# Kernel optimization log

Measured on AMD Instinct MI355X. Metric: run time of the kernel, lower is better.

The kernel has to match this reference:

```python
import jax, jax.numpy as jnp
import numpy as np

N, E, X_DIM, EA_DIM, HID, NL, NC, NGRAPH = 50000, 800000, 64, 16, 64, 3, 10, 64
BN_EPS = 1e-5
STD_EPS = 1e-5


def setup_inputs() -> dict:
    key = jax.random.key(0)
    ks = jax.random.split(key, 24)
    w = lambda k, sh: (jax.random.normal(k, sh, jnp.float32) * 0.05)
    inp = {
        'x': jax.random.normal(ks[0], (N, X_DIM), jnp.float32),
        'edge_index': jax.random.randint(ks[1], (2, E), 0, N),
        'batch': jnp.sort(jax.random.randint(ks[2], (N,), 0, NGRAPH)),
        'edge_attr': jax.random.normal(ks[3], (E, EA_DIM), jnp.float32),
        # node / edge encoders
        'node_w': w(ks[4], (X_DIM, HID)), 'node_b': jnp.zeros((HID,), jnp.float32),
        'edge_w': w(ks[5], (EA_DIM, HID)), 'edge_b': jnp.zeros((HID,), jnp.float32),
        # per-layer PNA post_nn Linear(12*3*HID -> HID) and BatchNorm
        'conv_w': w(ks[6], (NL, 12 * 3 * HID, HID)), 'conv_b': jnp.zeros((NL, HID), jnp.float32),
        'bn_g': jnp.ones((NL, HID), jnp.float32), 'bn_b': jnp.zeros((NL, HID), jnp.float32),
        # fc_out: HID -> HID/2 -> HID/4 -> NC
        'fc1_w': w(ks[7], (HID, HID // 2)), 'fc1_b': jnp.zeros((HID // 2,), jnp.float32),
        'fc2_w': w(ks[8], (HID // 2, HID // 4)), 'fc2_b': jnp.zeros((HID // 4,), jnp.float32),
        'fc3_w': w(ks[9], (HID // 4, NC)), 'fc3_b': jnp.zeros((NC,), jnp.float32),
    }
    return inp


def _pna_layer(x, src, dst, ea, deg, degc, log_deg, avg_log, w, b):
    # message: concat([x_i, x_j, edge_attr]) with x_i = x[dst], x_j = x[src]  -> [E, 3H]
    h = jnp.concatenate([x[dst], x[src], ea], axis=-1)
    inv = (1.0 / degc)[:, None]
    s1 = jax.ops.segment_sum(h, dst, num_segments=N)
    mean = s1 * inv
    mean_sq = jax.ops.segment_sum(h * h, dst, num_segments=N) * inv
    std = jnp.sqrt(jax.nn.relu(mean_sq - mean * mean) + STD_EPS)
    has = (deg > 0)[:, None]
    mx = jax.ops.segment_max(h, dst, num_segments=N)
    mx = jnp.where(has, mx, 0.0)
    mn = -jax.ops.segment_max(-h, dst, num_segments=N)
    mn = jnp.where(has, mn, 0.0)
    out = jnp.concatenate([mean, mn, mx, std], axis=-1)  # [N, 4*3H]
    amp = (log_deg / avg_log)[:, None]
    att = (avg_log / log_deg)[:, None]
    out = jnp.concatenate([out, out * amp, out * att], axis=-1)  # [N, 12*3H]
    return out @ w + b


def reference(x, edge_index, batch, edge_attr, node_w, node_b, edge_w, edge_b,
              conv_w, conv_b, bn_g, bn_b, fc1_w, fc1_b, fc2_w, fc2_b, fc3_w, fc3_b):
    src, dst = edge_index[0], edge_index[1]
    x = x @ node_w + node_b
    ea = edge_attr @ edge_w + edge_b
    deg = jax.ops.segment_sum(jnp.ones((E,), jnp.float32), dst, num_segments=N)
    degc = jnp.maximum(deg, 1.0)
    log_deg = jnp.log(degc + 1.0)
    # avg of log(deg+1) over nodes (equivalent to the histogram-based avg_deg['log'])
    avg_log = jnp.mean(jnp.log(deg + 1.0))
    for i in range(NL):
        h = _pna_layer(x, src, dst, ea, deg, degc, log_deg, avg_log, conv_w[i], conv_b[i])
        mu = jnp.mean(h, axis=0)
        var = jnp.mean((h - mu) ** 2, axis=0)  # biased var, as torch BN training mode
        h = (h - mu) * jax.lax.rsqrt(var + BN_EPS) * bn_g[i] + bn_b[i]
        x = jax.nn.relu(h) + x  # dropout is identity in eval
    # global mean pool over graphs
    gsum = jax.ops.segment_sum(x, batch, num_segments=NGRAPH)
    gcnt = jnp.maximum(jax.ops.segment_sum(jnp.ones((N,), jnp.float32), batch, num_segments=NGRAPH), 1.0)
    g = gsum / gcnt[:, None]
    g = jax.nn.relu(g @ fc1_w + fc1_b)
    g = jax.nn.relu(g @ fc2_w + fc2_b)
    return g @ fc3_w + fc3_b
```

## Files before the change

kernel.cpp:

```cpp
#include <hip/hip_runtime.h>
#include <math.h>

#define N_NODES 50000
#define N_EDGES 800000
#define NGRAPH  64
#define KEFF    576

typedef short bf16x8 __attribute__((ext_vector_type(8)));
typedef float f32x4  __attribute__((ext_vector_type(4)));
typedef unsigned int u32;
typedef unsigned int u32x4 __attribute__((ext_vector_type(4)));

__device__ inline unsigned short f2bf_rne(float f) {
  unsigned u = __float_as_uint(f);
  unsigned r = u + 0x7FFFu + ((u >> 16) & 1u);
  return (unsigned short)(r >> 16);
}
__device__ inline float bf2f(unsigned short h) {
  return __uint_as_float(((unsigned)h) << 16);
}

__device__ inline u32 cvtpk_bf16(float a, float b) {
  u32 r;
  asm("v_cvt_pk_bf16_f32 %0, %1, %2" : "=v"(r) : "v"(a), "v"(b));
  return r;
}

__device__ inline void split2(float a, float b, u32& ph, u32& pl) {
  ph = cvtpk_bf16(a, b);
  float ha = __uint_as_float(ph << 16);
  float hb = __uint_as_float(ph & 0xFFFF0000u);
  pl = cvtpk_bf16(a - ha, b - hb);
}

__device__ inline bf16x8 pack_bf(u32 w0, u32 w1, u32 w2, u32 w3) {
  u32x4 t;
  t.x = w0; t.y = w1; t.z = w2; t.w = w3;
  return __builtin_bit_cast(bf16x8, t);
}


__global__ __launch_bounds__(256) void zero_kernel(
    int* __restrict__ cnt, float* __restrict__ gsum,
    double* __restrict__ bnacc, double* __restrict__ avgacc)
{
  int i = blockIdx.x * 256 + threadIdx.x;
  if (i < N_NODES) { cnt[i] = 0; return; }
  int j = i - N_NODES;
  if (j < NGRAPH * 64) { gsum[j] = 0.f; return; }
  int k = j - NGRAPH * 64;
  if (k < 3 * 128) { bnacc[k] = 0.0; return; }
  if (k == 3 * 128) *avgacc = 0.0;
}

__global__ __launch_bounds__(256) void node_enc_kernel(
    const float* __restrict__ xin, const float* __restrict__ nw,
    const float* __restrict__ nb, float* __restrict__ x)
{
  __shared__ float xs[256];
  int tid = threadIdx.x;
  int base = blockIdx.x * 256;
  xs[tid] = xin[base + tid];
  __syncthreads();
  int r = tid >> 6, j = tid & 63;
  float acc = nb[j];
#pragma unroll
  for (int t = 0; t < 64; t++) acc = fmaf(xs[r * 64 + t], nw[t * 64 + j], acc);
  x[base + tid] = acc;
}

__global__ void count_kernel(const int* __restrict__ dst, int* __restrict__ cnt)
{
  int e = blockIdx.x * 256 + threadIdx.x;
  atomicAdd(&cnt[dst[e]], 1);
}

__global__ __launch_bounds__(256) void scan_a_kernel(
    const int* __restrict__ cnt, int* __restrict__ bsum)
{
  __shared__ int s[256];
  int i = blockIdx.x * 256 + threadIdx.x;
  s[threadIdx.x] = (i < N_NODES) ? cnt[i] : 0;
  __syncthreads();
  for (int off = 128; off > 0; off >>= 1) {
    if (threadIdx.x < off) s[threadIdx.x] += s[threadIdx.x + off];
    __syncthreads();
  }
  if (threadIdx.x == 0) bsum[blockIdx.x] = s[0];
}

__global__ __launch_bounds__(256) void scan_b_kernel(
    const int* __restrict__ bsum, int* __restrict__ boff)
{
  __shared__ int s[256];
  int tid = threadIdx.x;
  int v = (tid < 196) ? bsum[tid] : 0;
  s[tid] = v;
  __syncthreads();
  for (int off = 1; off < 256; off <<= 1) {
    int t = (tid >= off) ? s[tid - off] : 0;
    __syncthreads();
    s[tid] += t;
    __syncthreads();
  }
  boff[tid] = s[tid] - v;
}

__global__ __launch_bounds__(256) void scan_c_kernel(
    const int* __restrict__ cnt, const int* __restrict__ boff,
    int* __restrict__ row_ptr, int* __restrict__ cursor)
{
  __shared__ int s[256];
  int tid = threadIdx.x;
  int i = blockIdx.x * 256 + tid;
  int v = (i < N_NODES) ? cnt[i] : 0;
  s[tid] = v;
  __syncthreads();
  for (int off = 1; off < 256; off <<= 1) {
    int t = (tid >= off) ? s[tid - off] : 0;
    __syncthreads();
    s[tid] += t;
    __syncthreads();
  }
  int incl = s[tid];
  int base = boff[blockIdx.x];
  if (i < N_NODES) { row_ptr[i] = base + incl - v; cursor[i] = base + incl - v; }
  if (i == N_NODES - 1) row_ptr[N_NODES] = base + incl;
}

__global__ void fill_kernel(const int* __restrict__ src, const int* __restrict__ dst,
                            int* __restrict__ cursor, int* __restrict__ srcs,
                            int* __restrict__ eids)
{
  int e = blockIdx.x * 256 + threadIdx.x;
  int d = dst[e];
  int pos = atomicAdd(&cursor[d], 1);
  srcs[pos] = src[e];
  eids[pos] = e;
}

__global__ __launch_bounds__(256) void deg_log_kernel(
    const int* __restrict__ cnt, float* __restrict__ log_deg,
    double* __restrict__ avgacc)
{
  __shared__ double sb[256];
  int i = blockIdx.x * 256 + threadIdx.x;
  double c = 0.0;
  if (i < N_NODES) {
    int d = cnt[i];
    int dc = d > 0 ? d : 1;
    log_deg[i] = logf((float)dc + 1.0f);
    c = (double)logf((float)d + 1.0f);
  }
  sb[threadIdx.x] = c;
  __syncthreads();
  for (int off = 128; off > 0; off >>= 1) {
    if (threadIdx.x < off) sb[threadIdx.x] += sb[threadIdx.x + off];
    __syncthreads();
  }
  if (threadIdx.x == 0) atomicAdd(avgacc, sb[0]);
}

__global__ void avg_gb_kernel(const double* __restrict__ avgacc,
                              float* __restrict__ avgf,
                              const int* __restrict__ batch,
                              int* __restrict__ gcnt)
{
  __shared__ int sb[65];
  int g = threadIdx.x;
  int lo = 0, hi = N_NODES;
  while (lo < hi) { int mid = (lo + hi) >> 1; if (batch[mid] < g) lo = mid + 1; else hi = mid; }
  sb[g] = lo;
  if (g == 0) { sb[64] = N_NODES; *avgf = (float)(*avgacc / (double)N_NODES); }
  __syncthreads();
  gcnt[g] = sb[g + 1] - sb[g];
}


__global__ __launch_bounds__(256) void wprep_kernel(
    const float* __restrict__ conv_w, unsigned short* __restrict__ wh,
    unsigned short* __restrict__ wl)
{
  int idx = blockIdx.x * 256 + threadIdx.x;
  int k = idx % 576;
  int c = (idx / 576) % 192;
  int l = idx / (576 * 192);
  int s = c >> 6, j = c & 63;
  const float* CW = conv_w + (size_t)l * 2304 * 64;
  float v;
  if (k < 64) {
    int base = s * 768 + k;
    v = CW[base * 64 + j] + CW[(base + 192) * 64 + j] + CW[(base + 384) * 64 + j];
  } else {
    const int srcseg[8] = {1, 2, 4, 5, 7, 8, 10, 11};
    int q = (k >> 6) - 1;
    int t = k & 63;
    v = CW[(s * 768 + srcseg[q] * 64 + t) * 64 + j];
  }
  unsigned short hh = f2bf_rne(v);
  size_t o = (((size_t)l * 12 + (c >> 4)) * 72 + (k >> 3)) * 128 + (c & 15) * 8 + (k & 7);
  wh[o] = hh;
  wl[o] = f2bf_rne(v - bf2f(hh));
}

__global__ void bprep_kernel(const float* __restrict__ conv_w, float* __restrict__ beff)
{
  int l = blockIdx.x;
  int s = threadIdx.x >> 6, j = threadIdx.x & 63;
  const float* CW = conv_w + (size_t)l * 2304 * 64 + (size_t)(s * 768 + 576) * 64;
  float sum = 0.f;
#pragma unroll
  for (int t = 0; t < 64; t++) sum += CW[t * 64 + j];
  beff[(l * 3 + s) * 64 + j] = sum * 0.0031622776601683794f;
}

__global__ __launch_bounds__(256) void ewprep_kernel(
    const float* __restrict__ edge_w, unsigned short* __restrict__ ewh,
    unsigned short* __restrict__ ewl)
{
  int tid = threadIdx.x;
#pragma unroll
  for (int it = 0; it < 4; it++) {
    int idx = tid + 256 * it;
    int j = idx & 7, cb = (idx >> 3) & 3, l15 = (idx >> 5) & 15, hf = idx >> 9;
    float v = edge_w[(hf * 8 + j) * 64 + cb * 16 + l15];
    unsigned short h = f2bf_rne(v);
    ewh[idx] = h;
    ewl[idx] = f2bf_rne(v - bf2f(h));
  }
}


__device__ inline bf16x8 load_afrag(const float* __restrict__ eattr,
                                    const int* __restrict__ eids,
                                    int idx, int quad, bool wantlo)
{
  int eid = eids[idx];
  const float4* rp = (const float4*)(eattr + (size_t)eid * 16 + (quad & 1) * 8);
  float4 r0 = rp[0], r1 = rp[1];
  u32 h0, l0, h1, l1, h2, l2, h3, l3;
  split2(r0.x, r0.y, h0, l0);
  split2(r0.z, r0.w, h1, l1);
  split2(r1.x, r1.y, h2, l2);
  split2(r1.z, r1.w, h3, l3);
  return pack_bf(wantlo ? l0 : h0, wantlo ? l1 : h1,
                 wantlo ? l2 : h2, wantlo ? l3 : h3);
}

#define AGG_E_BLOCKS 2048
#define AGG_E_WAVES  (AGG_E_BLOCKS * 4)

__global__ __launch_bounds__(256) void agg_e_kernel(
    const float* __restrict__ eattr,
    const unsigned short* __restrict__ ewh, const unsigned short* __restrict__ ewl,
    const float* __restrict__ edge_b, const int* __restrict__ row_ptr,
    const int* __restrict__ eids,
    unsigned short* __restrict__ agg_h, unsigned short* __restrict__ agg_l)
{
  int lane = threadIdx.x & 63;
  int quad = lane >> 4, l15 = lane & 15;
  bool wantlo = quad >= 2;
  float eb = edge_b[lane];

  int fbase = ((quad & 1) * 16 + l15) * 32;
  bf16x8 wbh[4], wbl[4];
#pragma unroll
  for (int cb = 0; cb < 4; cb++) {
    wbh[cb] = *(const bf16x8*)(ewh + fbase + cb * 8);
    wbl[cb] = *(const bf16x8*)(ewl + fbase + cb * 8);
  }

  const f32x4 zero = {};
  for (int n = blockIdx.x * 4 + (threadIdx.x >> 6); n < N_NODES; n += AGG_E_WAVES) {
    int s0 = row_ptr[n], s1 = row_ptr[n + 1];
    float se[4] = {0.f, 0.f, 0.f, 0.f}, sq[4] = {0.f, 0.f, 0.f, 0.f};
    float mx[4], mn[4];
#pragma unroll
    for (int cb = 0; cb < 4; cb++) { mx[cb] = -3.4e38f; mn[cb] = 3.4e38f; }

    int j = s0;
    for (; j + 16 <= s1; j += 16) {
      bf16x8 af = load_afrag(eattr, eids, j + l15, quad, wantlo);
#pragma unroll
      for (int cb = 0; cb < 4; cb++) {
        f32x4 acc = __builtin_amdgcn_mfma_f32_16x16x32_bf16(af, wbh[cb], zero, 0, 0, 0);
        acc = __builtin_amdgcn_mfma_f32_16x16x32_bf16(af, wbl[cb], acc, 0, 0, 0);
#pragma unroll
        for (int r = 0; r < 4; r++) {
          float v = acc[r];
          se[cb] += v; sq[cb] = fmaf(v, v, sq[cb]);
          mx[cb] = fmaxf(mx[cb], v); mn[cb] = fminf(mn[cb], v);
        }
      }
    }
    if (j < s1) {
      int rem = s1 - j;
      int idx = j + l15; if (idx > s1 - 1) idx = s1 - 1;
      bf16x8 af = load_afrag(eattr, eids, idx, quad, wantlo);
#pragma unroll
      for (int cb = 0; cb < 4; cb++) {
        f32x4 acc = __builtin_amdgcn_mfma_f32_16x16x32_bf16(af, wbh[cb], zero, 0, 0, 0);
        acc = __builtin_amdgcn_mfma_f32_16x16x32_bf16(af, wbl[cb], acc, 0, 0, 0);
#pragma unroll
        for (int r = 0; r < 4; r++) {
          float v = acc[r];
          bool valid = (quad * 4 + r) < rem;
          float vm = valid ? v : 0.f;
          se[cb] += vm; sq[cb] = fmaf(vm, vm, sq[cb]);
          mx[cb] = fmaxf(mx[cb], v); mn[cb] = fminf(mn[cb], v);
        }
      }
    }

#pragma unroll
    for (int cb = 0; cb < 4; cb++) {
      se[cb] += __shfl_xor(se[cb], 16, 64); se[cb] += __shfl_xor(se[cb], 32, 64);
      sq[cb] += __shfl_xor(sq[cb], 16, 64); sq[cb] += __shfl_xor(sq[cb], 32, 64);
      mx[cb] = fmaxf(mx[cb], __shfl_xor(mx[cb], 16, 64));
      mx[cb] = fmaxf(mx[cb], __shfl_xor(mx[cb], 32, 64));
      mn[cb] = fminf(mn[cb], __shfl_xor(mn[cb], 16, 64));
      mn[cb] = fminf(mn[cb], __shfl_xor(mn[cb], 32, 64));
    }
    float SE = quad == 0 ? se[0] : quad == 1 ? se[1] : quad == 2 ? se[2] : se[3];
    float SQ = quad == 0 ? sq[0] : quad == 1 ? sq[1] : quad == 2 ? sq[2] : sq[3];
    float MX = quad == 0 ? mx[0] : quad == 1 ? mx[1] : quad == 2 ? mx[2] : mx[3];
    float MN = quad == 0 ? mn[0] : quad == 1 ? mn[1] : quad == 2 ? mn[2] : mn[3];

    int deg = s1 - s0;
    float inv = 1.0f / fmaxf((float)deg, 1.0f);
    bool has = deg > 0;
    float m0 = SE * inv, ms0 = SQ * inv;
    float sd_e = sqrtf(fmaxf(ms0 - m0 * m0, 0.f) + 1e-5f);
    float m_e = has ? m0 + eb : 0.f;
    float mx_e = has ? MX + eb : 0.f;
    float mn_e = has ? MN + eb : 0.f;

    unsigned short* bh = agg_h + (size_t)n * KEFF;
    unsigned short* bl = agg_l + (size_t)n * KEFF;
#define W2(off, val) { float _v = (val); unsigned short _h = f2bf_rne(_v); \
                       bh[(off) + lane] = _h; bl[(off) + lane] = f2bf_rne(_v - bf2f(_h)); }
    W2(128, m_e); W2(256, mn_e); W2(384, mx_e); W2(512, sd_e);
#undef W2
  }
}


__global__ __launch_bounds__(256) void agg_x_kernel(
    const float* __restrict__ x, const int* __restrict__ srcs,
    const int* __restrict__ row_ptr,
    unsigned short* __restrict__ agg_h, unsigned short* __restrict__ agg_l)
{
  int lane = threadIdx.x & 63;
  int n = blockIdx.x * 4 + (threadIdx.x >> 6);
  if (n >= N_NODES) return;
  float xd = x[(size_t)n * 64 + lane];
  int s0 = row_ptr[n], s1 = row_ptr[n + 1];
  float sA = 0.f, sB = 0.f, sC = 0.f, sD = 0.f;
  float qA = 0.f, qB = 0.f, qC = 0.f, qD = 0.f;
  float mx0 = -3.4e38f, mx1 = -3.4e38f, mn0 = 3.4e38f, mn1 = 3.4e38f;
  int j = s0;
  for (; j + 7 < s1; j += 8) {
    int e0 = srcs[j],     e1 = srcs[j + 1], e2 = srcs[j + 2], e3 = srcs[j + 3];
    int e4 = srcs[j + 4], e5 = srcs[j + 5], e6 = srcs[j + 6], e7 = srcs[j + 7];
    float x0 = x[(size_t)e0 * 64 + lane];
    float x1 = x[(size_t)e1 * 64 + lane];
    float x2 = x[(size_t)e2 * 64 + lane];
    float x3 = x[(size_t)e3 * 64 + lane];
    float x4 = x[(size_t)e4 * 64 + lane];
    float x5 = x[(size_t)e5 * 64 + lane];
    float x6 = x[(size_t)e6 * 64 + lane];
    float x7 = x[(size_t)e7 * 64 + lane];
    sA += x0; sB += x1; sC += x2; sD += x3;
    sA += x4; sB += x5; sC += x6; sD += x7;
    qA = fmaf(x0, x0, qA); qB = fmaf(x1, x1, qB);
    qC = fmaf(x2, x2, qC); qD = fmaf(x3, x3, qD);
    qA = fmaf(x4, x4, qA); qB = fmaf(x5, x5, qB);
    qC = fmaf(x6, x6, qC); qD = fmaf(x7, x7, qD);
    mx0 = fmaxf(mx0, fmaxf(fmaxf(x0, x1), fmaxf(x2, x3)));
    mx1 = fmaxf(mx1, fmaxf(fmaxf(x4, x5), fmaxf(x6, x7)));
    mn0 = fminf(mn0, fminf(fminf(x0, x1), fminf(x2, x3)));
    mn1 = fminf(mn1, fminf(fminf(x4, x5), fminf(x6, x7)));
  }
  if (j < s1) {
    int last = s1 - 1;
    int rem = s1 - j;
    int e0 = srcs[j];
    int e1 = srcs[j + 1 < s1 ? j + 1 : last];
    int e2 = srcs[j + 2 < s1 ? j + 2 : last];
    int e3 = srcs[j + 3 < s1 ? j + 3 : last];
    int e4 = srcs[j + 4 < s1 ? j + 4 : last];
    int e5 = srcs[j + 5 < s1 ? j + 5 : last];
    int e6 = srcs[j + 6 < s1 ? j + 6 : last];
    int e7 = srcs[j + 7 < s1 ? j + 7 : last];
    float x0 = x[(size_t)e0 * 64 + lane];
    float x1 = x[(size_t)e1 * 64 + lane];
    float x2 = x[(size_t)e2 * 64 + lane];
    float x3 = x[(size_t)e3 * 64 + lane];
    float x4 = x[(size_t)e4 * 64 + lane];
    float x5 = x[(size_t)e5 * 64 + lane];
    float x6 = x[(size_t)e6 * 64 + lane];
    float x7 = x[(size_t)e7 * 64 + lane];
    mx0 = fmaxf(mx0, fmaxf(fmaxf(x0, x1), fmaxf(x2, x3)));
    mx1 = fmaxf(mx1, fmaxf(fmaxf(x4, x5), fmaxf(x6, x7)));
    mn0 = fminf(mn0, fminf(fminf(x0, x1), fminf(x2, x3)));
    mn1 = fminf(mn1, fminf(fminf(x4, x5), fminf(x6, x7)));
    float z1 = 1 < rem ? x1 : 0.f;
    float z2 = 2 < rem ? x2 : 0.f;
    float z3 = 3 < rem ? x3 : 0.f;
    float z4 = 4 < rem ? x4 : 0.f;
    float z5 = 5 < rem ? x5 : 0.f;
    float z6 = 6 < rem ? x6 : 0.f;
    float z7 = 7 < rem ? x7 : 0.f;
    sA += x0; sB += z1; sC += z2; sD += z3;
    sA += z4; sB += z5; sC += z6; sD += z7;
    qA = fmaf(x0, x0, qA); qB = fmaf(z1, z1, qB);
    qC = fmaf(z2, z2, qC); qD = fmaf(z3, z3, qD);
    qA = fmaf(z4, z4, qA); qB = fmaf(z5, z5, qB);
    qC = fmaf(z6, z6, qC); qD = fmaf(z7, z7, qD);
  }
  float sx = (sA + sB) + (sC + sD);
  float qx = (qA + qB) + (qC + qD);
  float mxx = fmaxf(mx0, mx1), mnx = fminf(mn0, mn1);

  int deg = s1 - s0;
  float inv = 1.0f / fmaxf((float)deg, 1.0f);
  bool has = deg > 0;
  float m_s = sx * inv, ms_s = qx * inv;
  float sd_s = sqrtf(fmaxf(ms_s - m_s * m_s, 0.f) + 1e-5f);
  float mx_s = has ? mxx : 0.f, mn_s = has ? mnx : 0.f;

  unsigned short* bh = agg_h + (size_t)n * KEFF;
  unsigned short* bl = agg_l + (size_t)n * KEFF;
#define W2(off, val) { float _v = (val); unsigned short _h = f2bf_rne(_v); \
                       bh[(off) + lane] = _h; bl[(off) + lane] = f2bf_rne(_v - bf2f(_h)); }
  W2(0,   has ? xd : 0.f);
  W2(64,  m_s); W2(192, mn_s); W2(320, mx_s); W2(448, sd_s);
#undef W2
}


__global__ __launch_bounds__(256, 3) void gemm_kernel(
    const unsigned short* __restrict__ Ah, const unsigned short* __restrict__ Al,
    const unsigned short* __restrict__ Wh, const unsigned short* __restrict__ Wl,
    const float* __restrict__ beff, const float* __restrict__ bias,
    const float* __restrict__ log_deg, const float* __restrict__ avg_ptr,
    float* __restrict__ h, double* __restrict__ bnacc)
{
  __shared__ __align__(16) short AsH[64 * 40], AsL[64 * 40];
  int tid = threadIdx.x;
  int lane = tid & 63, w = tid >> 6;
  int quad = lane >> 4, l15 = lane & 15;
  int n0 = blockIdx.x * 64;

  int arow = tid >> 2, ac = tid & 3;
  int an = n0 + arow; if (an >= N_NODES) an = N_NODES - 1;
  const unsigned short* gah = Ah + (size_t)an * KEFF + ac * 8;
  const unsigned short* gal = Al + (size_t)an * KEFF + ac * 8;

  const unsigned short* pbh[3];
  const unsigned short* pbl[3];
#pragma unroll
  for (int s = 0; s < 3; s++) {
    size_t cb = (size_t)(s * 4 + w) * 72 * 128 + l15 * 8;
    pbh[s] = Wh + cb;
    pbl[s] = Wl + cb;
  }

  f32x4 acc[4][3] = {};
  float4 rh = *(const float4*)(gah);
  float4 rl = *(const float4*)(gal);

  for (int k0 = 0; k0 < KEFF; k0 += 32) {
    int koff = ((k0 >> 3) + quad) * 128;
    bf16x8 bhf[3], blf[3];
#pragma unroll
    for (int s = 0; s < 3; s++) {
      bhf[s] = *(const bf16x8*)(pbh[s] + koff);
      blf[s] = *(const bf16x8*)(pbl[s] + koff);
    }
    *(float4*)(AsH + arow * 40 + ac * 8) = rh;
    *(float4*)(AsL + arow * 40 + ac * 8) = rl;
    if (k0 + 32 < KEFF) {
      rh = *(const float4*)(gah + k0 + 32);
      rl = *(const float4*)(gal + k0 + 32);
    }
    __syncthreads();

#pragma unroll
    for (int i = 0; i < 4; i++) {
      int row = i * 16 + l15;
      bf16x8 ah = *(const bf16x8*)(AsH + row * 40 + quad * 8);
      bf16x8 al = *(const bf16x8*)(AsL + row * 40 + quad * 8);
#pragma unroll
      for (int s = 0; s < 3; s++) {
        acc[i][s] = __builtin_amdgcn_mfma_f32_16x16x32_bf16(ah, bhf[s], acc[i][s], 0, 0, 0);
        acc[i][s] = __builtin_amdgcn_mfma_f32_16x16x32_bf16(al, bhf[s], acc[i][s], 0, 0, 0);
        acc[i][s] = __builtin_amdgcn_mfma_f32_16x16x32_bf16(ah, blf[s], acc[i][s], 0, 0, 0);
      }
    }
    __syncthreads();
  }

  float avg = *avg_ptr;
  int col = w * 16 + l15;
  float be0 = beff[col], be1 = beff[64 + col], be2 = beff[128 + col];
  float bi = bias[col];
  float ss = 0.f, sq = 0.f;
#pragma unroll
  for (int i = 0; i < 4; i++) {
#pragma unroll
    for (int r = 0; r < 4; r++) {
      int n = n0 + i * 16 + quad * 4 + r;
      if (n < N_NODES) {
        float ld = log_deg[n];
        float amp = ld / avg, att = avg / ld;
        float v = (acc[i][0][r] + be0) + amp * (acc[i][1][r] + be1)
                + att * (acc[i][2][r] + be2) + bi;
        h[(size_t)n * 64 + col] = v;
        ss += v; sq = fmaf(v, v, sq);
      }
    }
  }
  ss += __shfl_xor(ss, 16, 64); ss += __shfl_xor(ss, 32, 64);
  sq += __shfl_xor(sq, 16, 64); sq += __shfl_xor(sq, 32, 64);
  if (quad == 0) {
    atomicAdd(&bnacc[col], (double)ss);
    atomicAdd(&bnacc[64 + col], (double)sq);
  }
}


__global__ __launch_bounds__(256) void apply_kernel(
    const float* __restrict__ h, const double* __restrict__ acc,
    const float* __restrict__ g, const float* __restrict__ bnb,
    float* __restrict__ x)
{
  __shared__ float smu[64], ssc[64];
  int tid = threadIdx.x;
  if (tid < 64) {
    double mu = acc[tid] / (double)N_NODES;
    double var = acc[64 + tid] / (double)N_NODES - mu * mu;
    double rstd = 1.0 / sqrt(var + 1e-5);
    smu[tid] = (float)mu;
    ssc[tid] = (float)(rstd * (double)g[tid]);
  }
  __syncthreads();
  int i4 = blockIdx.x * 256 + tid;
  const float4* h4 = (const float4*)h;
  float4* x4 = (float4*)x;
  int c4 = (i4 & 15) * 4;
  float4 hv = h4[i4], xv = x4[i4];
  float4 bb = ((const float4*)bnb)[i4 & 15];
  float4 r;
  r.x = fmaxf((hv.x - smu[c4])     * ssc[c4]     + bb.x, 0.f) + xv.x;
  r.y = fmaxf((hv.y - smu[c4 + 1]) * ssc[c4 + 1] + bb.y, 0.f) + xv.y;
  r.z = fmaxf((hv.z - smu[c4 + 2]) * ssc[c4 + 2] + bb.z, 0.f) + xv.z;
  r.w = fmaxf((hv.w - smu[c4 + 3]) * ssc[c4 + 3] + bb.w, 0.f) + xv.w;
  x4[i4] = r;
}


__global__ __launch_bounds__(256) void pool_kernel(
    const float* __restrict__ x, const int* __restrict__ batch,
    float* __restrict__ gsum)
{
  int tid = threadIdx.x;
  int j = tid & 63, ri = tid >> 6;
  float acc = 0.f; int cur = -1;
  for (int k = 0; k < 16; k++) {
    int n = blockIdx.x * 64 + k * 4 + ri;
    if (n < N_NODES) {
      int b = batch[n];
      if (b != cur) {
        if (cur >= 0) atomicAdd(&gsum[cur * 64 + j], acc);
        cur = b; acc = 0.f;
      }
      acc += x[(size_t)n * 64 + j];
    }
  }
  if (cur >= 0) atomicAdd(&gsum[cur * 64 + j], acc);
}

__global__ __launch_bounds__(64) void fc_kernel(
    const float* __restrict__ gsum, const int* __restrict__ gcnt,
    const float* __restrict__ w1, const float* __restrict__ b1,
    const float* __restrict__ w2, const float* __restrict__ b2,
    const float* __restrict__ w3, const float* __restrict__ b3,
    float* __restrict__ out)
{
  __shared__ float w1s[64 * 32], w2s[32 * 16], w3s[16 * 10];
  __shared__ float b1s[32], b2s[16], b3s[10];
  __shared__ float gvs[64], a1s[32], a2s[16];
  int g = blockIdx.x, tid = threadIdx.x;

#pragma unroll
  for (int i = 0; i < 32; i++) w1s[tid + 64 * i] = w1[tid + 64 * i];
#pragma unroll
  for (int i = 0; i < 8; i++)  w2s[tid + 64 * i] = w2[tid + 64 * i];
  { int i2 = tid; if (i2 < 160) w3s[i2] = w3[i2];
    i2 = tid + 64; if (i2 < 160) w3s[i2] = w3[i2];
    i2 = tid + 128; if (i2 < 160) w3s[i2] = w3[i2]; }
  if (tid < 32) b1s[tid] = b1[tid];
  if (tid < 16) b2s[tid] = b2[tid];
  if (tid < 10) b3s[tid] = b3[tid];
  float cnt = fmaxf((float)gcnt[g], 1.0f);
  gvs[tid] = gsum[g * 64 + tid] / cnt;
  __syncthreads();

  {
    int o = tid & 31, half = tid >> 5;
    float s = 0.f;
#pragma unroll
    for (int j = 0; j < 32; j++)
      s = fmaf(gvs[half * 32 + j], w1s[(half * 32 + j) * 32 + o], s);
    s += __shfl_xor(s, 32, 64);
    if (half == 0) a1s[o] = fmaxf(s + b1s[o], 0.f);
  }
  __syncthreads();

  {
    int o = tid & 15, part = tid >> 4;
    float s = 0.f;
#pragma unroll
    for (int j = 0; j < 8; j++)
      s = fmaf(a1s[part * 8 + j], w2s[(part * 8 + j) * 16 + o], s);
    s += __shfl_xor(s, 16, 64);
    s += __shfl_xor(s, 32, 64);
    if (part == 0) a2s[o] = fmaxf(s + b2s[o], 0.f);
  }
  __syncthreads();

  if (tid < 10) {
    float s = b3s[tid];
#pragma unroll
    for (int j = 0; j < 16; j++) s = fmaf(a2s[j], w3s[j * 10 + tid], s);
    out[g * 10 + tid] = s;
  }
}


extern "C" void kernel_launch(void* const* d_in, const int* in_sizes, int n_in,
                              void* d_out, int out_size, void* d_ws, size_t ws_size,
                              hipStream_t stream)
{
  (void)in_sizes; (void)n_in; (void)out_size; (void)ws_size;
  const float* xin    = (const float*)d_in[0];
  const int*   ei     = (const int*)d_in[1];
  const int*   batch  = (const int*)d_in[2];
  const float* eattr  = (const float*)d_in[3];
  const float* node_w = (const float*)d_in[4];
  const float* node_b = (const float*)d_in[5];
  const float* edge_w = (const float*)d_in[6];
  const float* edge_b = (const float*)d_in[7];
  const float* conv_w = (const float*)d_in[8];
  const float* conv_b = (const float*)d_in[9];
  const float* bn_g   = (const float*)d_in[10];
  const float* bn_b   = (const float*)d_in[11];
  const float* fc1_w  = (const float*)d_in[12];
  const float* fc1_b  = (const float*)d_in[13];
  const float* fc2_w  = (const float*)d_in[14];
  const float* fc2_b  = (const float*)d_in[15];
  const float* fc3_w  = (const float*)d_in[16];
  const float* fc3_b  = (const float*)d_in[17];
  float* out = (float*)d_out;
  const int* srcp = ei;
  const int* dstp = ei + N_EDGES;

  char* p = (char*)d_ws;
  auto alloc = [&](size_t b) { char* r = p; p += (b + 255) & ~(size_t)255; return (void*)r; };
  float*  x       = (float*)alloc((size_t)N_NODES * 64 * 4);
  float*  h       = (float*)alloc((size_t)N_NODES * 64 * 4);
  unsigned short* agg_h = (unsigned short*)alloc((size_t)N_NODES * KEFF * 2);
  unsigned short* agg_l = (unsigned short*)alloc((size_t)N_NODES * KEFF * 2);
  unsigned short* wh    = (unsigned short*)alloc((size_t)3 * 12 * 72 * 128 * 2);
  unsigned short* wl    = (unsigned short*)alloc((size_t)3 * 12 * 72 * 128 * 2);
  int*    srcs    = (int*)alloc((size_t)N_EDGES * 4);
  int*    eids    = (int*)alloc((size_t)N_EDGES * 4);
  float*  beff    = (float*)alloc((size_t)3 * 3 * 64 * 4);
  int*    row_ptr = (int*)alloc((N_NODES + 1) * 4);
  int*    cursor  = (int*)alloc((size_t)N_NODES * 4);
  int*    cnt     = (int*)alloc((size_t)N_NODES * 4);
  float*  log_deg = (float*)alloc((size_t)N_NODES * 4);
  int*    bsum    = (int*)alloc(256 * 4);
  int*    boff    = (int*)alloc(256 * 4);
  double* avgacc  = (double*)alloc(256);
  float*  avgf    = (float*)alloc(256);
  double* bnacc   = (double*)alloc(3 * 128 * 8);
  float*  gsum    = (float*)alloc((size_t)NGRAPH * 64 * 4);
  int*    gcnt    = (int*)alloc((size_t)NGRAPH * 4);
  unsigned short* ewh = (unsigned short*)alloc(1024 * 2);
  unsigned short* ewl = (unsigned short*)alloc(1024 * 2);

  zero_kernel<<<213, 256, 0, stream>>>(cnt, gsum, bnacc, avgacc);
  node_enc_kernel<<<12500, 256, 0, stream>>>(xin, node_w, node_b, x);
  count_kernel<<<3125, 256, 0, stream>>>(dstp, cnt);
  scan_a_kernel<<<196, 256, 0, stream>>>(cnt, bsum);
  scan_b_kernel<<<1, 256, 0, stream>>>(bsum, boff);
  scan_c_kernel<<<196, 256, 0, stream>>>(cnt, boff, row_ptr, cursor);
  fill_kernel<<<3125, 256, 0, stream>>>(srcp, dstp, cursor, srcs, eids);
  deg_log_kernel<<<196, 256, 0, stream>>>(cnt, log_deg, avgacc);
  avg_gb_kernel<<<1, 64, 0, stream>>>(avgacc, avgf, batch, gcnt);
  wprep_kernel<<<1296, 256, 0, stream>>>(conv_w, wh, wl);
  bprep_kernel<<<3, 192, 0, stream>>>(conv_w, beff);
  ewprep_kernel<<<1, 256, 0, stream>>>(edge_w, ewh, ewl);

  agg_e_kernel<<<AGG_E_BLOCKS, 256, 0, stream>>>(eattr, ewh, ewl, edge_b,
                                                 row_ptr, eids, agg_h, agg_l);

  for (int l = 0; l < 3; l++) {
    agg_x_kernel<<<12500, 256, 0, stream>>>(x, srcs, row_ptr, agg_h, agg_l);
    gemm_kernel<<<782, 256, 0, stream>>>(agg_h, agg_l,
                                         wh + (size_t)l * 12 * 72 * 128,
                                         wl + (size_t)l * 12 * 72 * 128,
                                         beff + l * 192, conv_b + l * 64,
                                         log_deg, avgf, h, bnacc + l * 128);
    apply_kernel<<<3125, 256, 0, stream>>>(h, bnacc + l * 128, bn_g + l * 64,
                                           bn_b + l * 64, x);
  }

  pool_kernel<<<782, 256, 0, stream>>>(x, batch, gsum);
  fc_kernel<<<NGRAPH, 64, 0, stream>>>(gsum, gcnt, fc1_w, fc1_b, fc2_w, fc2_b,
                                       fc3_w, fc3_b, out);
}
```

Measured before the change: 624.0 us.

## Use 32x32x16 MFMA for edge aggregation and prefetch two nodes' edges

Rewrites the edge-attribute aggregation kernel to use 32x32x16 bf16 MFMA tiles covering 32 edges per step, with the full hi/lo split done per lane (hi*hi + lo*hi + hi*lo) instead of the 16x16 variant. Each wave now handles a pair of nodes and issues both nodes' first edge loads up front to overlap memory latency. The weight fragment layout in the prep kernel changes to match. This cuts the cross-lane reductions and loop iterations per node, at the cost of more padded MFMA work for low-degree nodes and one extra MFMA per tile.

Result: faster. 603.3 us (median of 2 runs) (-3.3%).

```diff
diff --git a/kernel.cpp b/kernel.cpp
--- a/kernel.cpp
+++ b/kernel.cpp
@@ -8,6 +8,7 @@
 
 typedef short bf16x8 __attribute__((ext_vector_type(8)));
 typedef float f32x4  __attribute__((ext_vector_type(4)));
+typedef float f32x16 __attribute__((ext_vector_type(16)));
 typedef unsigned int u32;
 typedef unsigned int u32x4 __attribute__((ext_vector_type(4)));
 
@@ -222,30 +223,14 @@
 #pragma unroll
   for (int it = 0; it < 4; it++) {
     int idx = tid + 256 * it;
-    int j = idx & 7, cb = (idx >> 3) & 3, l15 = (idx >> 5) & 15, hf = idx >> 9;
-    float v = edge_w[(hf * 8 + j) * 64 + cb * 16 + l15];
+    int j = idx & 7, cb = (idx >> 3) & 1, l31 = (idx >> 4) & 31, hf = idx >> 9;
+    float v = edge_w[(hf * 8 + j) * 64 + cb * 32 + l31];
     unsigned short h = f2bf_rne(v);
     ewh[idx] = h;
     ewl[idx] = f2bf_rne(v - bf2f(h));
   }
 }
 
-
-__device__ inline bf16x8 load_afrag(const float* __restrict__ eattr,
-                                    const int* __restrict__ eids,
-                                    int idx, int quad, bool wantlo)
-{
-  int eid = eids[idx];
-  const float4* rp = (const float4*)(eattr + (size_t)eid * 16 + (quad & 1) * 8);
-  float4 r0 = rp[0], r1 = rp[1];
-  u32 h0, l0, h1, l1, h2, l2, h3, l3;
-  split2(r0.x, r0.y, h0, l0);
-  split2(r0.z, r0.w, h1, l1);
-  split2(r1.x, r1.y, h2, l2);
-  split2(r1.z, r1.w, h3, l3);
-  return pack_bf(wantlo ? l0 : h0, wantlo ? l1 : h1,
-                 wantlo ? l2 : h2, wantlo ? l3 : h3);
-}
 
 #define AGG_E_BLOCKS 2048
 #define AGG_E_WAVES  (AGG_E_BLOCKS * 4)
@@ -258,75 +243,65 @@
     unsigned short* __restrict__ agg_h, unsigned short* __restrict__ agg_l)
 {
   int lane = threadIdx.x & 63;
-  int quad = lane >> 4, l15 = lane & 15;
-  bool wantlo = quad >= 2;
+  int l31 = lane & 31, hf = lane >> 5;
   float eb = edge_b[lane];
 
-  int fbase = ((quad & 1) * 16 + l15) * 32;
-  bf16x8 wbh[4], wbl[4];
-#pragma unroll
-  for (int cb = 0; cb < 4; cb++) {
+  int fbase = (hf * 32 + l31) * 16;
+  bf16x8 wbh[2], wbl[2];
+#pragma unroll
+  for (int cb = 0; cb < 2; cb++) {
     wbh[cb] = *(const bf16x8*)(ewh + fbase + cb * 8);
     wbl[cb] = *(const bf16x8*)(ewl + fbase + cb * 8);
   }
 
-  const f32x4 zero = {};
-  for (int n = blockIdx.x * 4 + (threadIdx.x >> 6); n < N_NODES; n += AGG_E_WAVES) {
-    int s0 = row_ptr[n], s1 = row_ptr[n + 1];
-    float se[4] = {0.f, 0.f, 0.f, 0.f}, sq[4] = {0.f, 0.f, 0.f, 0.f};
-    float mx[4], mn[4];
-#pragma unroll
-    for (int cb = 0; cb < 4; cb++) { mx[cb] = -3.4e38f; mn[cb] = 3.4e38f; }
-
-    int j = s0;
-    for (; j + 16 <= s1; j += 16) {
-      bf16x8 af = load_afrag(eattr, eids, j + l15, quad, wantlo);
-#pragma unroll
-      for (int cb = 0; cb < 4; cb++) {
-        f32x4 acc = __builtin_amdgcn_mfma_f32_16x16x32_bf16(af, wbh[cb], zero, 0, 0, 0);
-        acc = __builtin_amdgcn_mfma_f32_16x16x32_bf16(af, wbl[cb], acc, 0, 0, 0);
-#pragma unroll
-        for (int r = 0; r < 4; r++) {
-          float v = acc[r];
-          se[cb] += v; sq[cb] = fmaf(v, v, sq[cb]);
-          mx[cb] = fmaxf(mx[cb], v); mn[cb] = fminf(mn[cb], v);
+  const f32x16 zero = {};
+  int wid = __builtin_amdgcn_readfirstlane(blockIdx.x * 4 + (threadIdx.x >> 6));
+
+  auto process = [&](int n, int s0, int s1, float4 d0, float4 d1) {
+    int deg = s1 - s0;
+    float se[2] = {0.f, 0.f}, sq[2] = {0.f, 0.f};
+    float mx[2] = {-3.4e38f, -3.4e38f}, mn[2] = {3.4e38f, 3.4e38f};
+    if (deg > 0) {
+      int j = s0;
+      while (true) {
+        int remh = (s1 - j) - 4 * hf;
+        u32 h0, l0, h1, l1, h2, l2, h3, l3;
+        split2(d0.x, d0.y, h0, l0); split2(d0.z, d0.w, h1, l1);
+        split2(d1.x, d1.y, h2, l2); split2(d1.z, d1.w, h3, l3);
+        bf16x8 ahi = pack_bf(h0, h1, h2, h3), alo = pack_bf(l0, l1, l2, l3);
+#pragma unroll
+        for (int cb = 0; cb < 2; cb++) {
+          f32x16 acc = __builtin_amdgcn_mfma_f32_32x32x16_bf16(ahi, wbh[cb], zero, 0, 0, 0);
+          acc = __builtin_amdgcn_mfma_f32_32x32x16_bf16(alo, wbh[cb], acc, 0, 0, 0);
+          acc = __builtin_amdgcn_mfma_f32_32x32x16_bf16(ahi, wbl[cb], acc, 0, 0, 0);
+#pragma unroll
+          for (int reg = 0; reg < 16; reg++) {
+            const int baserow = (reg & 3) + 8 * (reg >> 2);
+            float v = acc[reg];
+            float vm = (baserow < remh) ? v : 0.f;
+            se[cb] += vm; sq[cb] = fmaf(vm, vm, sq[cb]);
+            mx[cb] = fmaxf(mx[cb], v); mn[cb] = fminf(mn[cb], v);
+          }
         }
+        j += 32;
+        if (j >= s1) break;
+        int id = eids[min(j + l31, s1 - 1)];
+        const float4* pp = (const float4*)(eattr + (size_t)id * 16 + hf * 8);
+        d0 = pp[0]; d1 = pp[1];
       }
     }
-    if (j < s1) {
-      int rem = s1 - j;
-      int idx = j + l15; if (idx > s1 - 1) idx = s1 - 1;
-      bf16x8 af = load_afrag(eattr, eids, idx, quad, wantlo);
-#pragma unroll
-      for (int cb = 0; cb < 4; cb++) {
-        f32x4 acc = __builtin_amdgcn_mfma_f32_16x16x32_bf16(af, wbh[cb], zero, 0, 0, 0);
-        acc = __builtin_amdgcn_mfma_f32_16x16x32_bf16(af, wbl[cb], acc, 0, 0, 0);
-#pragma unroll
-        for (int r = 0; r < 4; r++) {
-          float v = acc[r];
-          bool valid = (quad * 4 + r) < rem;
-          float vm = valid ? v : 0.f;
-          se[cb] += vm; sq[cb] = fmaf(vm, vm, sq[cb]);
-          mx[cb] = fmaxf(mx[cb], v); mn[cb] = fminf(mn[cb], v);
-        }
-      }
-    }
-
-#pragma unroll
-    for (int cb = 0; cb < 4; cb++) {
-      se[cb] += __shfl_xor(se[cb], 16, 64); se[cb] += __shfl_xor(se[cb], 32, 64);
-      sq[cb] += __shfl_xor(sq[cb], 16, 64); sq[cb] += __shfl_xor(sq[cb], 32, 64);
-      mx[cb] = fmaxf(mx[cb], __shfl_xor(mx[cb], 16, 64));
+#pragma unroll
+    for (int cb = 0; cb < 2; cb++) {
+      se[cb] += __shfl_xor(se[cb], 32, 64);
+      sq[cb] += __shfl_xor(sq[cb], 32, 64);
       mx[cb] = fmaxf(mx[cb], __shfl_xor(mx[cb], 32, 64));
-      mn[cb] = fminf(mn[cb], __shfl_xor(mn[cb], 16, 64));
       mn[cb] = fminf(mn[cb], __shfl_xor(mn[cb], 32, 64));
     }
-    float SE = quad == 0 ? se[0] : quad == 1 ? se[1] : quad == 2 ? se[2] : se[3];
-    float SQ = quad == 0 ? sq[0] : quad == 1 ? sq[1] : quad == 2 ? sq[2] : sq[3];
-    float MX = quad == 0 ? mx[0] : quad == 1 ? mx[1] : quad == 2 ? mx[2] : mx[3];
-    float MN = quad == 0 ? mn[0] : quad == 1 ? mn[1] : quad == 2 ? mn[2] : mn[3];
-
-    int deg = s1 - s0;
+    float SE = hf ? se[1] : se[0];
+    float SQ = hf ? sq[1] : sq[0];
+    float MX = hf ? mx[1] : mx[0];
+    float MN = hf ? mn[1] : mn[0];
+
     float inv = 1.0f / fmaxf((float)deg, 1.0f);
     bool has = deg > 0;
     float m0 = SE * inv, ms0 = SQ * inv;
@@ -341,6 +316,25 @@
                        bh[(off) + lane] = _h; bl[(off) + lane] = f2bf_rne(_v - bf2f(_h)); }
     W2(128, m_e); W2(256, mn_e); W2(384, mx_e); W2(512, sd_e);
 #undef W2
+  };
+
+  for (int p = wid; p < N_NODES / 2; p += AGG_E_WAVES) {
+    int nA = 2 * p;
+    int r0 = row_ptr[nA], r1 = row_ptr[nA + 1], r2 = row_ptr[nA + 2];
+    int idA = 0, idB = 0;
+    if (r1 > r0) idA = eids[min(r0 + l31, r1 - 1)];
+    if (r2 > r1) idB = eids[min(r1 + l31, r2 - 1)];
+    float4 da0 = {}, da1 = {}, db0 = {}, db1 = {};
+    if (r1 > r0) {
+      const float4* pa = (const float4*)(eattr + (size_t)idA * 16 + hf * 8);
+      da0 = pa[0]; da1 = pa[1];
+    }
+    if (r2 > r1) {
+      const float4* pb = (const float4*)(eattr + (size_t)idB * 16 + hf * 8);
+      db0 = pb[0]; db1 = pb[1];
+    }
+    process(nA, r0, r1, da0, da1);
+    process(nA + 1, r1, r2, db0, db1);
   }
 }
 
```
